# Kernel optimization log

Hardware: AMD Instinct MI355X
Metric: run time of the kernel (lower is better)

The kernel has to match this reference:

```python
import jax, jax.numpy as jnp
import numpy as np

# Batched-graph dimensions: B graphs of N_PER_G nodes each (uniform sizes so
# the per-graph top-k is a fixed-shape lax.top_k over a [B, N_PER_G] reshape).
B = 256
N_PER_G = 2048
D = 128
DEG = 16
N = B * N_PER_G            # 524288 nodes
E = N * DEG                # 8388608 edges
RATIO = 0.5
K = int(N_PER_G * RATIO)   # nodes kept per graph


def setup_inputs() -> dict:
    key = jax.random.key(0)
    k1, k2, k3, k4, k5 = jax.random.split(key, 5)
    x = jax.random.normal(k1, (N, D), dtype=jnp.float32)
    # Random edges constrained to stay within each graph's node range.
    src_local = jax.random.randint(k2, (B, N_PER_G * DEG), 0, N_PER_G)
    dst_local = jax.random.randint(k3, (B, N_PER_G * DEG), 0, N_PER_G)
    offs = (jnp.arange(B) * N_PER_G)[:, None]
    edge_index = jnp.stack([(src_local + offs).reshape(-1),
                            (dst_local + offs).reshape(-1)], axis=0).astype(jnp.int32)
    edge_weight = jax.random.uniform(k4, (E,), dtype=jnp.float32)
    node_graph_index = jnp.repeat(jnp.arange(B, dtype=jnp.int32), N_PER_G)
    # score_gnn: single GCN layer projecting node features to a scalar score.
    W = (jax.random.normal(k5, (D, 1), dtype=jnp.float32) / np.sqrt(D)).astype(jnp.float32)
    return {"x": x, "edge_index": edge_index, "edge_weight": edge_weight,
            "node_graph_index": node_graph_index, "W": W}


def _gcn_score(x, edge_index, edge_weight, W):
    """Single GCN layer with renormalization (self-loops), output [N, 1]."""
    src, dst = edge_index[0], edge_index[1]
    deg = jax.ops.segment_sum(edge_weight, dst, num_segments=N) + 1.0  # +1 for self-loop
    inv_sqrt = jax.lax.rsqrt(deg)
    norm_w = edge_weight * inv_sqrt[src] * inv_sqrt[dst]      # [E]
    h = x @ W                                                 # [N, 1]
    out = jax.ops.segment_sum(norm_w[:, None] * h[src], dst, num_segments=N)
    out = out + h * (inv_sqrt * inv_sqrt)[:, None]            # self-loop term 1/deg
    return out


def reference(x, edge_index, edge_weight, node_graph_index, W):
    # 1. Score nodes with the score GNN.
    score = _gcn_score(x, edge_index, edge_weight, W)[:, 0]   # [N]
    # 2. Per-graph top-k (ratio-based): graphs are uniform size N_PER_G.
    _, local_idx = jax.lax.top_k(score.reshape(B, N_PER_G), K)        # [B, K]
    topk_index = (local_idx + (jnp.arange(B) * N_PER_G)[:, None]).reshape(-1)  # [B*K]
    # 3. Gate features by activated score, gather kept nodes.
    gated = x * jnp.tanh(score)[:, None]                      # [N, D]
    pooled_x = gated[topk_index]                              # [B*K, D]
    # 4. Reindex edges: keep edges with both endpoints retained, remap node ids.
    keep = jnp.zeros((N,), jnp.bool_).at[topk_index].set(True)
    new_id = jnp.zeros((N,), jnp.int32).at[topk_index].set(
        jnp.arange(B * K, dtype=jnp.int32))
    edge_mask = keep[edge_index[0]] & keep[edge_index[1]]     # [E]
    pooled_edge_index = jnp.where(edge_mask[None, :], new_id[edge_index], -1)
    pooled_edge_weight = jnp.where(edge_mask, edge_weight, 0.0)
    pooled_node_graph_index = node_graph_index[topk_index]
    return pooled_x, pooled_edge_index, pooled_edge_weight, pooled_node_graph_index
```

## Files before the change

kernel.cpp:

```cpp
#include <hip/hip_runtime.h>
#include <math.h>

#define NB   256
#define NPG  2048
#define DD   128
#define DEGC 16
#define NTOT (NB * NPG)
#define ETOT (NTOT * DEGC)
#define KK   (NPG / 2)
#define EPG  (NPG * DEGC)
#define NCB  16
#define CBN  128
#define CAP  2560

__global__ __launch_bounds__(256) void k_h(const float* __restrict__ x,
                                           const float* __restrict__ W,
                                           float* __restrict__ h) {
    int lane = threadIdx.x & 63;
    int wv   = threadIdx.x >> 6;
    int half = lane >> 5;
    int sub  = lane & 31;
    int node = blockIdx.x * 8 + wv * 2 + half;
    const float4* x4 = (const float4*)x;
    const float4* W4 = (const float4*)W;
    float4 xv = x4[(size_t)node * 32 + sub];
    float4 wv4 = W4[sub];
    float p = xv.x * wv4.x + xv.y * wv4.y + xv.z * wv4.z + xv.w * wv4.w;
    #pragma unroll
    for (int off = 16; off >= 1; off >>= 1) p += __shfl_xor(p, off, 64);
    if (sub == 0) h[node] = p;
}

__global__ __launch_bounds__(1024) void k_part(const int* __restrict__ src,
                                               const int* __restrict__ dst,
                                               const float* __restrict__ w,
                                               int* __restrict__ cptr_g,
                                               int* __restrict__ ccnt_g,
                                               float2* __restrict__ ebws,
                                               int* __restrict__ ebe) {
    int g = blockIdx.x, t = threadIdx.x;
    __shared__ int ccnt[NCB];
    __shared__ int ccur[NCB];
    const int*   dslab = dst + (size_t)g * EPG;
    const int*   sslab = src + (size_t)g * EPG;
    const float* wslab = w   + (size_t)g * EPG;
    if (t < NCB) ccnt[t] = 0;
    __syncthreads();
    int dloc[EPG / 1024];
    #pragma unroll
    for (int i = 0; i < EPG / 1024; i++) {
        dloc[i] = dslab[i * 1024 + t] - g * NPG;
        atomicAdd(&ccnt[dloc[i] >> 7], 1);
    }
    __syncthreads();
    if (t == 0) {
        int acc = 0;
        for (int b = 0; b < NCB; b++) {
            int c = ccnt[b];
            cptr_g[g * NCB + b] = acc;
            ccnt_g[g * NCB + b] = c;
            ccur[b] = acc;
            acc += c;
        }
    }
    __syncthreads();
    size_t gb = (size_t)g * EPG;
    #pragma unroll
    for (int i = 0; i < EPG / 1024; i++) {
        int e = i * 1024 + t;
        int d = dloc[i];
        int pos = atomicAdd(&ccur[d >> 7], 1);
        ebe[gb + pos] = (e << 7) | (d & 127);
        float2 r;
        r.x = wslab[e];
        r.y = __int_as_float(sslab[e] - g * NPG);
        ebws[gb + pos] = r;
    }
}

__global__ __launch_bounds__(256) void k_fine(const int* __restrict__ cptr_g,
                                              const int* __restrict__ ccnt_g,
                                              float2* ebws,
                                              const int* __restrict__ ebe,
                                              int* __restrict__ ptr,
                                              int* __restrict__ cnt,
                                              float* __restrict__ is_arr) {
    __shared__ int   skey[CAP];
    __shared__ float sw[CAP];
    __shared__ float sy[CAP];
    __shared__ int cnt_f[CBN];
    __shared__ int cur_f[CBN];
    __shared__ int base_f[CBN];
    __shared__ int tmp[CBN];
    int g = blockIdx.x >> 4, cb = blockIdx.x & 15, t = threadIdx.x;
    int cb_base = cptr_g[g * NCB + cb];
    int ncb     = ccnt_g[g * NCB + cb];
    size_t gb = (size_t)g * EPG + cb_base;
    if (t < CBN) cnt_f[t] = 0;
    __syncthreads();
    for (int i = t; i < ncb; i += 256) atomicAdd(&cnt_f[ebe[gb + i] & 127], 1);
    __syncthreads();
    if (t < CBN) tmp[t] = cnt_f[t];
    __syncthreads();
    for (int off = 1; off < CBN; off <<= 1) {
        int v = 0;
        if (t < CBN && t >= off) v = tmp[t - off];
        __syncthreads();
        if (t < CBN) tmp[t] += v;
        __syncthreads();
    }
    if (t < CBN) { base_f[t] = (t ? tmp[t - 1] : 0); cur_f[t] = base_f[t]; }
    __syncthreads();
    for (int i = t; i < ncb; i += 256) {
        int ev = ebe[gb + i];
        int f  = ev & 127;
        int pos = atomicAdd(&cur_f[f], 1);
        if (pos < CAP) {
            float2 r = ebws[gb + i];
            skey[pos] = ((ev >> 7) << 12) | pos;
            sw[pos] = r.x;
            sy[pos] = r.y;
        }
    }
    __syncthreads();
    if (t < CBN) {
        int b0 = base_f[t], k = cnt_f[t];
        for (int i = 1; i < k; i++) {
            int v = skey[b0 + i];
            int j = i - 1;
            while (j >= 0) {
                int u = skey[b0 + j];
                if (u > v) { skey[b0 + j + 1] = u; j--; } else break;
            }
            skey[b0 + j + 1] = v;
        }
        float s = 0.0f;
        for (int i = 0; i < k; i++) s += sw[skey[b0 + i] & 4095];
        float deg = s + 1.0f;
        int node = g * NPG + cb * CBN + t;
        is_arr[node] = 1.0f / sqrtf(deg);
        ptr[node] = (int)gb + b0;
        cnt[node] = k;
    }
    __syncthreads();
    for (int i = t; i < ncb; i += 256) {
        int idx = skey[i] & 4095;
        float2 r;
        r.x = sw[idx];
        r.y = sy[idx];
        ebws[gb + i] = r;
    }
}

__global__ __launch_bounds__(256) void k_score(const int* __restrict__ ptr,
                                               const int* __restrict__ cnt,
                                               const float2* __restrict__ pwsrc,
                                               const float* __restrict__ h,
                                               const float* __restrict__ is_arr,
                                               float* __restrict__ score) {
    __shared__ float sh_h[NPG];
    __shared__ float sh_is[NPG];
    int b = blockIdx.x >> 3;
    for (int i = threadIdx.x; i < NPG; i += 256) {
        sh_h[i]  = h[(size_t)b * NPG + i];
        sh_is[i] = is_arr[(size_t)b * NPG + i];
    }
    __syncthreads();
    int n = blockIdx.x * 256 + threadIdx.x;
    int nl = n & (NPG - 1);
    int beg = ptr[n], k = cnt[n];
    float isd = sh_is[nl];
    float s = 0.0f;
    for (int i = 0; i < k; i++) {
        float2 r = pwsrc[beg + i];
        int sl = __float_as_int(r.y);
        float v = ((r.x * sh_is[sl]) * isd) * sh_h[sl];
        s += v;
    }
    s = s + sh_h[nl] * (isd * isd);
    score[n] = s;
}

__global__ __launch_bounds__(1024) void k_topk(const float* __restrict__ score,
                                               int* __restrict__ topk,
                                               int* __restrict__ new_id,
                                               float* __restrict__ pngi) {
    int b = blockIdx.x, t = threadIdx.x;
    __shared__ unsigned long long key[NPG];
    for (int i = t; i < NPG; i += 1024) {
        float s = score[b * NPG + i];
        unsigned int u = __float_as_uint(s);
        u = (u & 0x80000000u) ? ~u : (u | 0x80000000u);
        unsigned int ks = ~u;
        key[i] = ((unsigned long long)ks << 32) | (unsigned int)i;
    }
    __syncthreads();
    for (int k = 2; k <= NPG; k <<= 1) {
        for (int j = k >> 1; j > 0; j >>= 1) {
            int i = ((t & ~(j - 1)) << 1) | (t & (j - 1));
            int p = i | j;
            bool up = ((i & k) == 0);
            unsigned long long a = key[i], c = key[p];
            if ((a > c) == up) { key[i] = c; key[p] = a; }
            __syncthreads();
        }
    }
    int local = (int)(key[t] & 0xFFFFFFFFu);
    int node = b * NPG + local;
    int j = b * KK + t;
    topk[j] = node;
    new_id[node] = j;
    pngi[j] = (float)b;
}

__global__ __launch_bounds__(256) void k_gather(const float* __restrict__ x,
                                                const float* __restrict__ score,
                                                const int* __restrict__ topk,
                                                float* __restrict__ out) {
    int q = blockIdx.x * 256 + threadIdx.x;
    int row = q >> 5, c = q & 31;
    int node = topk[row];
    float g = tanhf(score[node]);
    const float4* x4 = (const float4*)x;
    float4 v = x4[(size_t)node * 32 + c];
    float4 o;
    o.x = v.x * g; o.y = v.y * g; o.z = v.z * g; o.w = v.w * g;
    ((float4*)out)[q] = o;
}

__global__ __launch_bounds__(256) void k_edges(const int* __restrict__ src,
                                               const int* __restrict__ dst,
                                               const float* __restrict__ w,
                                               const int* __restrict__ new_id,
                                               float* __restrict__ pei0,
                                               float* __restrict__ pei1,
                                               float* __restrict__ pew) {
    int e = blockIdx.x * 256 + threadIdx.x;
    int s = src[e], d = dst[e];
    int ns = new_id[s], nd = new_id[d];
    bool m = (ns >= 0) && (nd >= 0);
    pei0[e] = m ? (float)ns : -1.0f;
    pei1[e] = m ? (float)nd : -1.0f;
    pew[e]  = m ? w[e] : 0.0f;
}

extern "C" void kernel_launch(void* const* d_in, const int* in_sizes, int n_in,
                              void* d_out, int out_size, void* d_ws, size_t ws_size,
                              hipStream_t stream) {
    const float* x   = (const float*)d_in[0];
    const int*   ei  = (const int*)d_in[1];
    const float* w   = (const float*)d_in[2];
    const float* W   = (const float*)d_in[4];
    const int* src = ei;
    const int* dst = ei + ETOT;

    char* ws = (char*)d_ws;
    float*  h      = (float*)(ws);
    float*  is_arr = h + NTOT;
    float*  score  = is_arr + NTOT;
    int*    cnt    = (int*)(score + NTOT);
    int*    ptr    = cnt + NTOT;
    int*    new_id = ptr + NTOT;
    int*    topk   = new_id + NTOT;
    int*    ebe    = topk + (size_t)NB * KK;
    float2* ebws   = (float2*)(ebe + (size_t)ETOT);
    int* cptr_g = topk;
    int* ccnt_g = topk + NB * NCB;

    float* out_px   = (float*)d_out;
    float* out_pei0 = out_px + (size_t)NB * KK * DD;
    float* out_pei1 = out_pei0 + ETOT;
    float* out_pew  = out_pei1 + ETOT;
    float* out_pngi = out_pew + ETOT;

    hipMemsetAsync(new_id, 0xFF, (size_t)NTOT * 4, stream);

    k_h<<<NTOT / 8, 256, 0, stream>>>(x, W, h);
    k_part<<<NB, 1024, 0, stream>>>(src, dst, w, cptr_g, ccnt_g, ebws, ebe);
    k_fine<<<NB * NCB, 256, 0, stream>>>(cptr_g, ccnt_g, ebws, ebe, ptr, cnt, is_arr);
    k_score<<<NTOT / 256, 256, 0, stream>>>(ptr, cnt, ebws, h, is_arr, score);
    k_topk<<<NB, 1024, 0, stream>>>(score, topk, new_id, out_pngi);
    k_gather<<<(NB * KK * DD / 4) / 256, 256, 0, stream>>>(x, score, topk, out_px);
    k_edges<<<ETOT / 256, 256, 0, stream>>>(src, dst, w, new_id, out_pei0, out_pei1, out_pew);
}
```

Baseline: 793.4 us.

## Fuse score, top-k, gather and edge reindex into one per-graph kernel

Merges the score, top-k sort, gated gather and edge remap kernels into a single kernel with one 1024-thread block per graph. Scores stay in registers and shared memory, the tanh gate is recovered from the sort key, and new ids live in a shared per-graph table, so the global memset and the score/new_id/topk round-trips go away. The cost is that only 256 blocks do all the bandwidth-heavy gather and edge work, which may leave the GPU under-occupied compared with the earlier wide grids.

```diff
diff --git a/kernel.cpp b/kernel.cpp
--- a/kernel.cpp
+++ b/kernel.cpp
@@ -152,47 +152,55 @@
     }
 }
 
-__global__ __launch_bounds__(256) void k_score(const int* __restrict__ ptr,
-                                               const int* __restrict__ cnt,
-                                               const float2* __restrict__ pwsrc,
-                                               const float* __restrict__ h,
-                                               const float* __restrict__ is_arr,
-                                               float* __restrict__ score) {
+__global__ __launch_bounds__(1024) void k_final(const int* __restrict__ ptr,
+                                                const int* __restrict__ cnt,
+                                                const float2* __restrict__ pwsrc,
+                                                const float* __restrict__ h,
+                                                const float* __restrict__ is_arr,
+                                                const float* __restrict__ x,
+                                                const int* __restrict__ src,
+                                                const int* __restrict__ dst,
+                                                const float* __restrict__ w,
+                                                float* __restrict__ out_px,
+                                                float* __restrict__ out_pei0,
+                                                float* __restrict__ out_pei1,
+                                                float* __restrict__ out_pew,
+                                                float* __restrict__ out_pngi) {
     __shared__ float sh_h[NPG];
     __shared__ float sh_is[NPG];
-    int b = blockIdx.x >> 3;
-    for (int i = threadIdx.x; i < NPG; i += 256) {
-        sh_h[i]  = h[(size_t)b * NPG + i];
-        sh_is[i] = is_arr[(size_t)b * NPG + i];
-    }
-    __syncthreads();
-    int n = blockIdx.x * 256 + threadIdx.x;
-    int nl = n & (NPG - 1);
-    int beg = ptr[n], k = cnt[n];
-    float isd = sh_is[nl];
-    float s = 0.0f;
-    for (int i = 0; i < k; i++) {
-        float2 r = pwsrc[beg + i];
-        int sl = __float_as_int(r.y);
-        float v = ((r.x * sh_is[sl]) * isd) * sh_h[sl];
-        s += v;
-    }
-    s = s + sh_h[nl] * (isd * isd);
-    score[n] = s;
-}
-
-__global__ __launch_bounds__(1024) void k_topk(const float* __restrict__ score,
-                                               int* __restrict__ topk,
-                                               int* __restrict__ new_id,
-                                               float* __restrict__ pngi) {
-    int b = blockIdx.x, t = threadIdx.x;
     __shared__ unsigned long long key[NPG];
+    __shared__ int new_local[NPG];
+    int g = blockIdx.x, t = threadIdx.x;
     for (int i = t; i < NPG; i += 1024) {
-        float s = score[b * NPG + i];
-        unsigned int u = __float_as_uint(s);
+        sh_h[i]  = h[(size_t)g * NPG + i];
+        sh_is[i] = is_arr[(size_t)g * NPG + i];
+    }
+    __syncthreads();
+    float sc[2];
+    #pragma unroll
+    for (int r = 0; r < 2; r++) {
+        int nl = t + r * 1024;
+        int n = g * NPG + nl;
+        int beg = ptr[n], k = cnt[n];
+        float isd = sh_is[nl];
+        float s = 0.0f;
+        for (int i = 0; i < k; i++) {
+            float2 rr = pwsrc[beg + i];
+            int sl = __float_as_int(rr.y);
+            float v = ((rr.x * sh_is[sl]) * isd) * sh_h[sl];
+            s += v;
+        }
+        sc[r] = s + sh_h[nl] * (isd * isd);
+    }
+    __syncthreads();
+    #pragma unroll
+    for (int r = 0; r < 2; r++) {
+        int nl = t + r * 1024;
+        unsigned int u = __float_as_uint(sc[r]);
         u = (u & 0x80000000u) ? ~u : (u | 0x80000000u);
         unsigned int ks = ~u;
-        key[i] = ((unsigned long long)ks << 32) | (unsigned int)i;
+        key[nl] = ((unsigned long long)ks << 32) | (unsigned int)nl;
+        new_local[nl] = -1;
     }
     __syncthreads();
     for (int k = 2; k <= NPG; k <<= 1) {
@@ -205,43 +213,36 @@
             __syncthreads();
         }
     }
-    int local = (int)(key[t] & 0xFFFFFFFFu);
-    int node = b * NPG + local;
-    int j = b * KK + t;
-    topk[j] = node;
-    new_id[node] = j;
-    pngi[j] = (float)b;
-}
-
-__global__ __launch_bounds__(256) void k_gather(const float* __restrict__ x,
-                                                const float* __restrict__ score,
-                                                const int* __restrict__ topk,
-                                                float* __restrict__ out) {
-    int q = blockIdx.x * 256 + threadIdx.x;
-    int row = q >> 5, c = q & 31;
-    int node = topk[row];
-    float g = tanhf(score[node]);
+    {
+        int local = (int)(key[t] & 0xFFFFFFFFu);
+        new_local[local] = t;
+        out_pngi[g * KK + t] = (float)g;
+    }
+    __syncthreads();
     const float4* x4 = (const float4*)x;
-    float4 v = x4[(size_t)node * 32 + c];
-    float4 o;
-    o.x = v.x * g; o.y = v.y * g; o.z = v.z * g; o.w = v.w * g;
-    ((float4*)out)[q] = o;
-}
-
-__global__ __launch_bounds__(256) void k_edges(const int* __restrict__ src,
-                                               const int* __restrict__ dst,
-                                               const float* __restrict__ w,
-                                               const int* __restrict__ new_id,
-                                               float* __restrict__ pei0,
-                                               float* __restrict__ pei1,
-                                               float* __restrict__ pew) {
-    int e = blockIdx.x * 256 + threadIdx.x;
-    int s = src[e], d = dst[e];
-    int ns = new_id[s], nd = new_id[d];
-    bool m = (ns >= 0) && (nd >= 0);
-    pei0[e] = m ? (float)ns : -1.0f;
-    pei1[e] = m ? (float)nd : -1.0f;
-    pew[e]  = m ? w[e] : 0.0f;
+    float4* o4 = (float4*)out_px;
+    for (int q = t; q < KK * (DD / 4); q += 1024) {
+        int row = q >> 5, c = q & 31;
+        unsigned long long kk = key[row];
+        int local = (int)(kk & 0xFFFFFFFFu);
+        unsigned int u = ~(unsigned int)(kk >> 32);
+        unsigned int orig = (u & 0x80000000u) ? (u ^ 0x80000000u) : ~u;
+        float gm = tanhf(__uint_as_float(orig));
+        float4 xv = x4[((size_t)g * NPG + local) * 32 + c];
+        float4 o;
+        o.x = xv.x * gm; o.y = xv.y * gm; o.z = xv.z * gm; o.w = xv.w * gm;
+        o4[((size_t)g * KK + row) * 32 + c] = o;
+    }
+    size_t eb = (size_t)g * EPG;
+    for (int e = t; e < EPG; e += 1024) {
+        int sl = src[eb + e] - g * NPG;
+        int dl = dst[eb + e] - g * NPG;
+        int ns = new_local[sl], nd = new_local[dl];
+        bool m = (ns >= 0) && (nd >= 0);
+        out_pei0[eb + e] = m ? (float)(g * KK + ns) : -1.0f;
+        out_pei1[eb + e] = m ? (float)(g * KK + nd) : -1.0f;
+        out_pew[eb + e]  = m ? w[eb + e] : 0.0f;
+    }
 }
 
 extern "C" void kernel_launch(void* const* d_in, const int* in_sizes, int n_in,
@@ -257,15 +258,15 @@
     char* ws = (char*)d_ws;
     float*  h      = (float*)(ws);
     float*  is_arr = h + NTOT;
-    float*  score  = is_arr + NTOT;
-    int*    cnt    = (int*)(score + NTOT);
+    float*  score_dead = is_arr + NTOT;
+    int*    cnt    = (int*)(score_dead + NTOT);
     int*    ptr    = cnt + NTOT;
-    int*    new_id = ptr + NTOT;
-    int*    topk   = new_id + NTOT;
-    int*    ebe    = topk + (size_t)NB * KK;
+    int*    new_id_dead = ptr + NTOT;
+    int*    tkreg  = new_id_dead + NTOT;
+    int*    ebe    = tkreg + (size_t)NB * KK;
     float2* ebws   = (float2*)(ebe + (size_t)ETOT);
-    int* cptr_g = topk;
-    int* ccnt_g = topk + NB * NCB;
+    int* cptr_g = tkreg;
+    int* ccnt_g = tkreg + NB * NCB;
 
     float* out_px   = (float*)d_out;
     float* out_pei0 = out_px + (size_t)NB * KK * DD;
@@ -273,13 +274,9 @@
     float* out_pew  = out_pei1 + ETOT;
     float* out_pngi = out_pew + ETOT;
 
-    hipMemsetAsync(new_id, 0xFF, (size_t)NTOT * 4, stream);
-
     k_h<<<NTOT / 8, 256, 0, stream>>>(x, W, h);
     k_part<<<NB, 1024, 0, stream>>>(src, dst, w, cptr_g, ccnt_g, ebws, ebe);
     k_fine<<<NB * NCB, 256, 0, stream>>>(cptr_g, ccnt_g, ebws, ebe, ptr, cnt, is_arr);
-    k_score<<<NTOT / 256, 256, 0, stream>>>(ptr, cnt, ebws, h, is_arr, score);
-    k_topk<<<NB, 1024, 0, stream>>>(score, topk, new_id, out_pngi);
-    k_gather<<<(NB * KK * DD / 4) / 256, 256, 0, stream>>>(x, score, topk, out_px);
-    k_edges<<<ETOT / 256, 256, 0, stream>>>(src, dst, w, new_id, out_pei0, out_pei1, out_pew);
-}
+    k_final<<<NB, 1024, 0, stream>>>(ptr, cnt, ebws, h, is_arr, x, src, dst, w,
+                                     out_px, out_pei0, out_pei1, out_pew, out_pngi);
+}
```

After: 778.3 us. No clear change (-1.9%).
